# Kernel tuning notes

Measured on AMD Instinct MI355X. Metric: run time of the kernel, lower is better.

The kernel has to match this reference:

```python
import jax, jax.numpy as jnp
import numpy as np

DIM = 768
NUM_HEADS = 12
HEAD_DIM = DIM // NUM_HEADS
SCALE = HEAD_DIM ** -0.5


def setup_inputs() -> dict:
    key = jax.random.key(0)
    k_x, k_qw, k_qb, k_pw, k_pb = jax.random.split(key, 5)
    B, S = 4, 2048
    x = jax.random.normal(k_x, (B, S, DIM), dtype=jnp.float32)
    # torch nn.Linear convention: weight shape [out_features, in_features]
    qkv_w = jax.random.normal(k_qw, (2 * DIM, DIM), dtype=jnp.float32) * 0.02
    qkv_b = jax.random.normal(k_qb, (2 * DIM,), dtype=jnp.float32) * 0.02
    proj_w = jax.random.normal(k_pw, (DIM, DIM), dtype=jnp.float32) * 0.02
    proj_b = jax.random.normal(k_pb, (DIM,), dtype=jnp.float32) * 0.02
    return {"x": x, "qkv_w": qkv_w, "qkv_b": qkv_b, "proj_w": proj_w, "proj_b": proj_b}


def reference(x, qkv_w, qkv_b, proj_w, proj_b):
    B, S, D = x.shape
    H, Hd = NUM_HEADS, HEAD_DIM
    # qkv projection -> (B, S, 2*D)
    qkv = jnp.einsum('bsd,ed->bse', x, qkv_w) + qkv_b
    # reshape to (B, S, 2, H, Hd) then split q, v with heads leading: (B, H, S, Hd)
    qkv = qkv.reshape(B, S, 2, H, Hd).transpose(2, 0, 3, 1, 4)
    q, v = qkv[0], qkv[1]
    q = q * SCALE
    # shared Q=K scores: (B, H, S, S)
    attn = jnp.einsum('bhid,bhjd->bhij', q, q)
    attn = jax.nn.softmax(attn, axis=-1)  # attn_drop p=0 (identity)
    out = jnp.einsum('bhij,bhjd->bhid', attn, v)
    out = out.transpose(0, 2, 1, 3).reshape(B, S, D)
    out = jnp.einsum('bsd,ed->bse', out, proj_w) + proj_b  # proj_drop p=0
    return out
```

## Files before the change

### kernel.cpp

```cpp
#include <hip/hip_runtime.h>
#include <hip/hip_bf16.h>

#define NH 12
#define HD 64
#define SEQ 2048
#define DM 768

typedef __attribute__((ext_vector_type(8))) short bf16x8;
typedef __attribute__((ext_vector_type(4))) short bf16x4;
typedef __attribute__((ext_vector_type(4))) float f32x4;

static __device__ __forceinline__ unsigned short f2bf(float f) {
  unsigned int u = __float_as_uint(f);
  u += 0x7fff + ((u >> 16) & 1);
  return (unsigned short)(u >> 16);
}

static __device__ __forceinline__ unsigned cvt_pk_bf16(float lo, float hi) {
  unsigned r;
  asm("v_cvt_pk_bf16_f32 %0, %1, %2" : "=v"(r) : "v"(lo), "v"(hi));
  return r;
}

static __device__ __forceinline__ void gload_lds16(const void* g, void* l) {
  __builtin_amdgcn_global_load_lds(
      (const __attribute__((address_space(1))) void*)g,
      (__attribute__((address_space(3))) void*)l, 16, 0, 0);
}

static __device__ __forceinline__ f32x4 mfma16(bf16x4 a, bf16x4 b, f32x4 c) {
#if __has_builtin(__builtin_amdgcn_mfma_f32_16x16x16bf16_1k)
  return __builtin_amdgcn_mfma_f32_16x16x16bf16_1k(a, b, c, 0, 0, 0);
#elif __has_builtin(__builtin_amdgcn_mfma_f32_16x16x16_bf16)
  return __builtin_amdgcn_mfma_f32_16x16x16_bf16(a, b, c, 0, 0, 0);
#else
  asm("v_mfma_f32_16x16x16_bf16 %0, %1, %2, %0" : "+v"(c) : "v"(a), "v"(b));
  return c;
#endif
}

#define QSCALE 0.15014030f

__global__ __launch_bounds__(256) void cvt3_kernel(
    const float* __restrict__ s0, unsigned short* __restrict__ d0, int n0,
    const float* __restrict__ s1, unsigned short* __restrict__ d1, int n1,
    const float* __restrict__ s2, unsigned short* __restrict__ d2, int n2) {
  int i = blockIdx.x * 256 + threadIdx.x;
  const int stride = gridDim.x * 256;
  const int ntot = n0 + n1 + n2;
  for (; i < ntot; i += stride) {
    const float* src;
    unsigned short* dst;
    int j = i;
    if (j < n0) { src = s0; dst = d0; }
    else if (j < n0 + n1) { j -= n0; src = s1; dst = d1; }
    else { j -= n0 + n1; src = s2; dst = d2; }
    const float4 a = reinterpret_cast<const float4*>(src)[j * 2];
    const float4 b = reinterpret_cast<const float4*>(src)[j * 2 + 1];
    ushort4 lo = make_ushort4(f2bf(a.x), f2bf(a.y), f2bf(a.z), f2bf(a.w));
    ushort4 hi = make_ushort4(f2bf(b.x), f2bf(b.y), f2bf(b.z), f2bf(b.w));
    reinterpret_cast<ushort4*>(dst)[j * 2] = lo;
    reinterpret_cast<ushort4*>(dst)[j * 2 + 1] = hi;
  }
}

__global__ __launch_bounds__(256) void qkv_kernel(
    const unsigned short* __restrict__ xb, const unsigned short* __restrict__ wb,
    const float* __restrict__ bias,
    unsigned short* __restrict__ qb, unsigned short* __restrict__ vtb) {
  __shared__ alignas(16) char As[2][8192];
  __shared__ alignas(16) char Bs[2][8192];
  const int tid = threadIdx.x;
  const int lane = tid & 63, wid = tid >> 6;
  const int wr = wid >> 1, wc = wid & 1;
  const int g = lane >> 4, c = lane & 15;
  const int m0 = blockIdx.x * 128, n0 = blockIdx.y * 128;
  const char* Ab = (const char*)xb;
  const char* Bb = (const char*)wb;

  const int o0 = tid * 16, o1 = tid * 16 + 4096;
  const int r0 = o0 >> 6, r1 = o1 >> 6;
  const int sw0 = (o0 & 63) ^ (((r0 >> 1) & 3) << 4);
  const int sw1 = (o1 & 63) ^ (((r1 >> 1) & 3) << 4);

  auto stage = [&](int kt, int buf) {
    const int k0b = kt * 64;
    gload_lds16(Ab + (size_t)(m0 + r0) * 1536 + k0b + sw0, &As[buf][o0]);
    gload_lds16(Bb + (size_t)(n0 + r0) * 1536 + k0b + sw0, &Bs[buf][o0]);
    gload_lds16(Ab + (size_t)(m0 + r1) * 1536 + k0b + sw1, &As[buf][o1]);
    gload_lds16(Bb + (size_t)(n0 + r1) * 1536 + k0b + sw1, &Bs[buf][o1]);
  };

  f32x4 acc[4][4] = {};
  stage(0, 0);

  for (int kt = 0; kt < 24; ++kt) {
    __syncthreads();
    if (kt < 23) stage(kt + 1, (kt + 1) & 1);
    const char* Ap = As[kt & 1];
    const char* Bp = Bs[kt & 1];
    bf16x8 a_f[4], b_f[4];
#pragma unroll
    for (int i = 0; i < 4; ++i) {
      const int ra = wr * 64 + i * 16 + c;
      const int rb = wc * 64 + i * 16 + c;
      a_f[i] = *reinterpret_cast<const bf16x8*>(Ap + ra * 64 + ((g ^ ((ra >> 1) & 3)) << 4));
      b_f[i] = *reinterpret_cast<const bf16x8*>(Bp + rb * 64 + ((g ^ ((rb >> 1) & 3)) << 4));
    }
#pragma unroll
    for (int ai = 0; ai < 4; ++ai)
#pragma unroll
      for (int ni = 0; ni < 4; ++ni)
        acc[ai][ni] = __builtin_amdgcn_mfma_f32_16x16x32_bf16(a_f[ai], b_f[ni], acc[ai][ni], 0, 0, 0);
  }

#pragma unroll
  for (int ni = 0; ni < 4; ++ni) {
    const int n = n0 + wc * 64 + ni * 16 + c;
    const float bn = bias[n];
    if (n < DM) {
      const int h = n >> 6, d = n & 63;
#pragma unroll
      for (int ai = 0; ai < 4; ++ai)
#pragma unroll
        for (int r = 0; r < 4; ++r) {
          const int m = m0 + wr * 64 + ai * 16 + g * 4 + r;
          const int bb = m >> 11, s = m & 2047;
          qb[(((size_t)(bb * NH + h)) * SEQ + s) * HD + d] = f2bf((acc[ai][ni][r] + bn) * QSCALE);
        }
    } else {
      const int nn = n - DM;
      const int h = nn >> 6, d = nn & 63;
#pragma unroll
      for (int ai = 0; ai < 4; ++ai) {
        const int m_base = m0 + wr * 64 + ai * 16 + g * 4;
        const int bb = m_base >> 11, s0 = m_base & 2047;
        ushort4 pk = make_ushort4(f2bf(acc[ai][ni][0] + bn), f2bf(acc[ai][ni][1] + bn),
                                  f2bf(acc[ai][ni][2] + bn), f2bf(acc[ai][ni][3] + bn));
        *reinterpret_cast<ushort4*>(
            &vtb[((size_t)(bb * NH + h) * HD + d) * SEQ + s0]) = pk;
      }
    }
  }
}

__global__ __launch_bounds__(256, 4) void attn_kernel(
    const unsigned short* __restrict__ qb, const unsigned short* __restrict__ vtb,
    unsigned short* __restrict__ ao) {
  __shared__ alignas(16) char pool[2][16384];

  const int tid = threadIdx.x;
  const int lane = tid & 63, wid = tid >> 6;
  const int g = lane >> 4, c = lane & 15;
  const int wq = wid >> 1, wk = wid & 1;

  const int wg = blockIdx.x;
  const int xcd = wg & 7;
  const int idx = wg >> 3;
  const int bh = xcd * 6 + (idx >> 5);
  const int qs0 = (idx & 31) * 64;
  const size_t base = (size_t)bh * SEQ * HD;

  bf16x8 qf[2][2];
#pragma unroll
  for (int jq = 0; jq < 2; ++jq) {
    const unsigned short* qrow = &qb[base + (size_t)(qs0 + wq * 32 + jq * 16 + c) * HD + g * 8];
    qf[jq][0] = *reinterpret_cast<const bf16x8*>(qrow);
    qf[jq][1] = *reinterpret_cast<const bf16x8*>(qrow + 32);
  }

  const char* qbB = (const char*)qb;
  const char* vtB = (const char*)vtb;
  const int oK0 = tid * 16, oK1 = tid * 16 + 4096;
  const int swK0 = oK0 ^ (((oK0 >> 7) & 7) << 4);
  const int swK1 = oK1 ^ (((oK1 >> 7) & 7) << 4);
  const int oV0 = tid * 16, oV1 = tid * 16 + 4096;
  const int rV0 = oV0 >> 7, rV1 = oV1 >> 7;
  const int swV0 = (oV0 & 127) ^ (((rV0) & 7) << 4);
  const int swV1 = (oV1 & 127) ^ (((rV1) & 7) << 4);

  auto stage = [&](int t, int buf) {
    char* P = pool[buf];
    const size_t kQ = base * 2 + (size_t)t * 8192;
    gload_lds16(qbB + kQ + swK0, P + oK0);
    gload_lds16(qbB + kQ + swK1, P + oK1);
    gload_lds16(vtB + ((size_t)(bh * HD + rV0) * SEQ + t * 64) * 2 + swV0, P + 8192 + oV0);
    gload_lds16(vtB + ((size_t)(bh * HD + rV1) * SEQ + t * 64) * 2 + swV1, P + 8192 + oV1);
  };

  float l_p[2] = {0.f, 0.f};
  f32x4 o_acc[4][2] = {};

  const int cswz = (c & 7) << 4;

  stage(0, 0);
  asm volatile("s_waitcnt vmcnt(0)" ::: "memory");
  __builtin_amdgcn_sched_barrier(0);
  __builtin_amdgcn_s_barrier();

  for (int t = 0; t < 32; ++t) {
    const char* P = pool[t & 1];
    if (t < 31) stage(t + 1, (t + 1) & 1);

    f32x4 sa[2][2] = {};
    __builtin_amdgcn_s_setprio(1);
#pragma unroll
    for (int jp = 0; jp < 2; ++jp) {
      const int krow = wk * 32 + jp * 16 + c;
      const bf16x8 kf0 = *reinterpret_cast<const bf16x8*>(P + krow * 128 + ((g * 16) ^ cswz));
      const bf16x8 kf1 = *reinterpret_cast<const bf16x8*>(P + krow * 128 + ((64 + g * 16) ^ cswz));
#pragma unroll
      for (int jq = 0; jq < 2; ++jq) {
        sa[jp][jq] = __builtin_amdgcn_mfma_f32_16x16x32_bf16(kf0, qf[jq][0], sa[jp][jq], 0, 0, 0);
        sa[jp][jq] = __builtin_amdgcn_mfma_f32_16x16x32_bf16(kf1, qf[jq][1], sa[jp][jq], 0, 0, 0);
      }
    }
    __builtin_amdgcn_s_setprio(0);

    bf16x4 pb[2][2];
#pragma unroll
    for (int jp = 0; jp < 2; ++jp)
#pragma unroll
      for (int jq = 0; jq < 2; ++jq) {
        float p0 = __builtin_amdgcn_exp2f(sa[jp][jq][0]);
        float p1 = __builtin_amdgcn_exp2f(sa[jp][jq][1]);
        float p2 = __builtin_amdgcn_exp2f(sa[jp][jq][2]);
        float p3 = __builtin_amdgcn_exp2f(sa[jp][jq][3]);
        l_p[jq] += (p0 + p1) + (p2 + p3);
        uint2 wv = make_uint2(cvt_pk_bf16(p0, p1), cvt_pk_bf16(p2, p3));
        pb[jp][jq] = *reinterpret_cast<bf16x4*>(&wv);
      }

    __builtin_amdgcn_s_setprio(1);
#pragma unroll
    for (int dn = 0; dn < 4; ++dn) {
      const int vrow = dn * 16 + c;
      const bf16x4 vf0 = *reinterpret_cast<const bf16x4*>(
          P + 8192 + vrow * 128 + ((wk * 64 + 8 * g) ^ cswz));
      const bf16x4 vf1 = *reinterpret_cast<const bf16x4*>(
          P + 8192 + vrow * 128 + ((wk * 64 + 32 + 8 * g) ^ cswz));
#pragma unroll
      for (int jq = 0; jq < 2; ++jq) {
        o_acc[dn][jq] = mfma16(vf0, pb[0][jq], o_acc[dn][jq]);
        o_acc[dn][jq] = mfma16(vf1, pb[1][jq], o_acc[dn][jq]);
      }
    }
    __builtin_amdgcn_s_setprio(0);

    asm volatile("s_waitcnt vmcnt(0)" ::: "memory");
    __builtin_amdgcn_sched_barrier(0);
    __builtin_amdgcn_s_barrier();
  }

#pragma unroll
  for (int jq = 0; jq < 2; ++jq) {
    float v = l_p[jq];
    v += __shfl_xor(v, 16);
    v += __shfl_xor(v, 32);
    l_p[jq] = v;
  }

  float* ex = (float*)(pool[0] + wq * 16384);
  float* exl = ex + 32 * 68;
  if (wk == 1) {
#pragma unroll
    for (int dn = 0; dn < 4; ++dn)
#pragma unroll
      for (int jq = 0; jq < 2; ++jq)
        *reinterpret_cast<f32x4*>(&ex[(jq * 16 + c) * 68 + dn * 16 + 4 * g]) = o_acc[dn][jq];
    if (g == 0) {
      exl[c] = l_p[0];
      exl[16 + c] = l_p[1];
    }
  }
  __syncthreads();
  if (wk == 0) {
    const int b = bh / NH, h = bh % NH;
    float linv[2];
#pragma unroll
    for (int jq = 0; jq < 2; ++jq)
      linv[jq] = __builtin_amdgcn_rcpf(l_p[jq] + exl[jq * 16 + c]);
#pragma unroll
    for (int dn = 0; dn < 4; ++dn)
#pragma unroll
      for (int jq = 0; jq < 2; ++jq) {
        f32x4 o = o_acc[dn][jq];
        o += *reinterpret_cast<const f32x4*>(&ex[(jq * 16 + c) * 68 + dn * 16 + 4 * g]);
        uint2 wv = make_uint2(cvt_pk_bf16(o[0] * linv[jq], o[1] * linv[jq]),
                              cvt_pk_bf16(o[2] * linv[jq], o[3] * linv[jq]));
        *reinterpret_cast<uint2*>(
            &ao[((size_t)b * SEQ + qs0 + wq * 32 + jq * 16 + c) * DM + h * HD + dn * 16 + 4 * g]) = wv;
      }
  }
}

__global__ __launch_bounds__(256) void proj_kernel(
    const unsigned short* __restrict__ ao, const unsigned short* __restrict__ pwb,
    const float* __restrict__ bias, float* __restrict__ out) {
  __shared__ alignas(16) char As[2][8192];
  __shared__ alignas(16) char Bs[2][8192];
  const int tid = threadIdx.x;
  const int lane = tid & 63, wid = tid >> 6;
  const int wr = wid >> 1, wc = wid & 1;
  const int g = lane >> 4, c = lane & 15;
  const int m0 = blockIdx.x * 128, n0 = blockIdx.y * 128;
  const char* Ab = (const char*)ao;
  const char* Bb = (const char*)pwb;

  const int o0 = tid * 16, o1 = tid * 16 + 4096;
  const int r0 = o0 >> 6, r1 = o1 >> 6;
  const int sw0 = (o0 & 63) ^ (((r0 >> 1) & 3) << 4);
  const int sw1 = (o1 & 63) ^ (((r1 >> 1) & 3) << 4);

  auto stage = [&](int kt, int buf) {
    const int k0b = kt * 64;
    gload_lds16(Ab + (size_t)(m0 + r0) * 1536 + k0b + sw0, &As[buf][o0]);
    gload_lds16(Bb + (size_t)(n0 + r0) * 1536 + k0b + sw0, &Bs[buf][o0]);
    gload_lds16(Ab + (size_t)(m0 + r1) * 1536 + k0b + sw1, &As[buf][o1]);
    gload_lds16(Bb + (size_t)(n0 + r1) * 1536 + k0b + sw1, &Bs[buf][o1]);
  };

  f32x4 acc[4][4] = {};
  stage(0, 0);

  for (int kt = 0; kt < 24; ++kt) {
    __syncthreads();
    if (kt < 23) stage(kt + 1, (kt + 1) & 1);
    const char* Ap = As[kt & 1];
    const char* Bp = Bs[kt & 1];
    bf16x8 a_f[4], b_f[4];
#pragma unroll
    for (int i = 0; i < 4; ++i) {
      const int ra = wr * 64 + i * 16 + c;
      const int rb = wc * 64 + i * 16 + c;
      a_f[i] = *reinterpret_cast<const bf16x8*>(Ap + ra * 64 + ((g ^ ((ra >> 1) & 3)) << 4));
      b_f[i] = *reinterpret_cast<const bf16x8*>(Bp + rb * 64 + ((g ^ ((rb >> 1) & 3)) << 4));
    }
#pragma unroll
    for (int ai = 0; ai < 4; ++ai)
#pragma unroll
      for (int ni = 0; ni < 4; ++ni)
        acc[ai][ni] = __builtin_amdgcn_mfma_f32_16x16x32_bf16(a_f[ai], b_f[ni], acc[ai][ni], 0, 0, 0);
  }

#pragma unroll
  for (int ni = 0; ni < 4; ++ni) {
    const int n = n0 + wc * 64 + ni * 16 + c;
    const float bn = bias[n];
#pragma unroll
    for (int ai = 0; ai < 4; ++ai)
#pragma unroll
      for (int r = 0; r < 4; ++r) {
        const int m = m0 + wr * 64 + ai * 16 + g * 4 + r;
        out[(size_t)m * DM + n] = acc[ai][ni][r] + bn;
      }
  }
}

extern "C" void kernel_launch(void* const* d_in, const int* in_sizes, int n_in,
                              void* d_out, int out_size, void* d_ws, size_t ws_size,
                              hipStream_t stream) {
  const float* x = (const float*)d_in[0];
  const float* qkv_w = (const float*)d_in[1];
  const float* qkv_b = (const float*)d_in[2];
  const float* proj_w = (const float*)d_in[3];
  const float* proj_b = (const float*)d_in[4];
  float* out = (float*)d_out;

  const size_t elems = (size_t)4 * NH * SEQ * HD;
  unsigned short* qbuf = (unsigned short*)d_ws;
  unsigned short* vtbuf = qbuf + elems;
  unsigned short* xbf = vtbuf + elems;
  unsigned short* aobuf = xbf;
  unsigned short* wqkvbf = xbf + elems;
  unsigned short* wprojbf = wqkvbf + (size_t)2 * DM * DM;

  cvt3_kernel<<<dim3(2048), 256, 0, stream>>>(
      x, xbf, (int)(elems / 8),
      qkv_w, wqkvbf, 2 * DM * DM / 8,
      proj_w, wprojbf, DM * DM / 8);

  qkv_kernel<<<dim3(64, 12), 256, 0, stream>>>(xbf, wqkvbf, qkv_b, qbuf, vtbuf);
  attn_kernel<<<dim3(1536), 256, 0, stream>>>(qbuf, vtbuf, aobuf);
  proj_kernel<<<dim3(64, 6), 256, 0, stream>>>(aobuf, wprojbf, proj_b, out);
}
```

Baseline: 132.9 us.

## Split attention key tile across four waves with 512-thread blocks

Doubles the attention block to 512 threads so each wave handles 16 keys of every 64-key tile instead of 32. Each thread now issues one K and one V async load per stage instead of two. The four partial O accumulators and row sums are reduced through LDS in three serialized rounds. This raises wave-level parallelism and memory-issue concurrency per block, at the cost of more barriers in the epilogue and a heavier occupancy constraint from the launch bounds.

```diff
diff --git a/kernel.cpp b/kernel.cpp
--- a/kernel.cpp
+++ b/kernel.cpp
@@ -144,15 +144,16 @@
   }
 }
 
-__global__ __launch_bounds__(256, 4) void attn_kernel(
+__global__ __launch_bounds__(512, 6) void attn_kernel(
     const unsigned short* __restrict__ qb, const unsigned short* __restrict__ vtb,
     unsigned short* __restrict__ ao) {
   __shared__ alignas(16) char pool[2][16384];
+  __shared__ alignas(16) float lsum[4][64];
 
   const int tid = threadIdx.x;
   const int lane = tid & 63, wid = tid >> 6;
   const int g = lane >> 4, c = lane & 15;
-  const int wq = wid >> 1, wk = wid & 1;
+  const int wq = wid >> 2, wk = wid & 3;
 
   const int wg = blockIdx.x;
   const int xcd = wg & 7;
@@ -171,27 +172,22 @@
 
   const char* qbB = (const char*)qb;
   const char* vtB = (const char*)vtb;
-  const int oK0 = tid * 16, oK1 = tid * 16 + 4096;
-  const int swK0 = oK0 ^ (((oK0 >> 7) & 7) << 4);
-  const int swK1 = oK1 ^ (((oK1 >> 7) & 7) << 4);
-  const int oV0 = tid * 16, oV1 = tid * 16 + 4096;
-  const int rV0 = oV0 >> 7, rV1 = oV1 >> 7;
-  const int swV0 = (oV0 & 127) ^ (((rV0) & 7) << 4);
-  const int swV1 = (oV1 & 127) ^ (((rV1) & 7) << 4);
+  const int oT = tid * 16;
+  const int swK = oT ^ (((oT >> 7) & 7) << 4);
+  const int rV = oT >> 7;
+  const int swV = (oT & 127) ^ ((rV & 7) << 4);
 
   auto stage = [&](int t, int buf) {
     char* P = pool[buf];
-    const size_t kQ = base * 2 + (size_t)t * 8192;
-    gload_lds16(qbB + kQ + swK0, P + oK0);
-    gload_lds16(qbB + kQ + swK1, P + oK1);
-    gload_lds16(vtB + ((size_t)(bh * HD + rV0) * SEQ + t * 64) * 2 + swV0, P + 8192 + oV0);
-    gload_lds16(vtB + ((size_t)(bh * HD + rV1) * SEQ + t * 64) * 2 + swV1, P + 8192 + oV1);
+    gload_lds16(qbB + base * 2 + (size_t)t * 8192 + swK, P + oT);
+    gload_lds16(vtB + ((size_t)(bh * HD + rV) * SEQ + t * 64) * 2 + swV, P + 8192 + oT);
   };
 
   float l_p[2] = {0.f, 0.f};
   f32x4 o_acc[4][2] = {};
 
-  const int cswz = (c & 7) << 4;
+  const int krow = wk * 16 + c;
+  const int kswz = (c & 7) << 4;
 
   stage(0, 0);
   asm volatile("s_waitcnt vmcnt(0)" ::: "memory");
@@ -202,48 +198,40 @@
     const char* P = pool[t & 1];
     if (t < 31) stage(t + 1, (t + 1) & 1);
 
-    f32x4 sa[2][2] = {};
-    __builtin_amdgcn_s_setprio(1);
-#pragma unroll
-    for (int jp = 0; jp < 2; ++jp) {
-      const int krow = wk * 32 + jp * 16 + c;
-      const bf16x8 kf0 = *reinterpret_cast<const bf16x8*>(P + krow * 128 + ((g * 16) ^ cswz));
-      const bf16x8 kf1 = *reinterpret_cast<const bf16x8*>(P + krow * 128 + ((64 + g * 16) ^ cswz));
+    f32x4 sa[2] = {};
+    {
+      const bf16x8 kf0 = *reinterpret_cast<const bf16x8*>(P + krow * 128 + ((g * 16) ^ kswz));
+      const bf16x8 kf1 = *reinterpret_cast<const bf16x8*>(P + krow * 128 + ((64 + g * 16) ^ kswz));
+      __builtin_amdgcn_s_setprio(1);
 #pragma unroll
       for (int jq = 0; jq < 2; ++jq) {
-        sa[jp][jq] = __builtin_amdgcn_mfma_f32_16x16x32_bf16(kf0, qf[jq][0], sa[jp][jq], 0, 0, 0);
-        sa[jp][jq] = __builtin_amdgcn_mfma_f32_16x16x32_bf16(kf1, qf[jq][1], sa[jp][jq], 0, 0, 0);
+        sa[jq] = __builtin_amdgcn_mfma_f32_16x16x32_bf16(kf0, qf[jq][0], sa[jq], 0, 0, 0);
+        sa[jq] = __builtin_amdgcn_mfma_f32_16x16x32_bf16(kf1, qf[jq][1], sa[jq], 0, 0, 0);
       }
-    }
-    __builtin_amdgcn_s_setprio(0);
-
-    bf16x4 pb[2][2];
-#pragma unroll
-    for (int jp = 0; jp < 2; ++jp)
-#pragma unroll
-      for (int jq = 0; jq < 2; ++jq) {
-        float p0 = __builtin_amdgcn_exp2f(sa[jp][jq][0]);
-        float p1 = __builtin_amdgcn_exp2f(sa[jp][jq][1]);
-        float p2 = __builtin_amdgcn_exp2f(sa[jp][jq][2]);
-        float p3 = __builtin_amdgcn_exp2f(sa[jp][jq][3]);
-        l_p[jq] += (p0 + p1) + (p2 + p3);
-        uint2 wv = make_uint2(cvt_pk_bf16(p0, p1), cvt_pk_bf16(p2, p3));
-        pb[jp][jq] = *reinterpret_cast<bf16x4*>(&wv);
-      }
+      __builtin_amdgcn_s_setprio(0);
+    }
+
+    bf16x4 pb[2];
+#pragma unroll
+    for (int jq = 0; jq < 2; ++jq) {
+      float p0 = __builtin_amdgcn_exp2f(sa[jq][0]);
+      float p1 = __builtin_amdgcn_exp2f(sa[jq][1]);
+      float p2 = __builtin_amdgcn_exp2f(sa[jq][2]);
+      float p3 = __builtin_amdgcn_exp2f(sa[jq][3]);
+      l_p[jq] += (p0 + p1) + (p2 + p3);
+      uint2 wv = make_uint2(cvt_pk_bf16(p0, p1), cvt_pk_bf16(p2, p3));
+      pb[jq] = *reinterpret_cast<bf16x4*>(&wv);
+    }
 
     __builtin_amdgcn_s_setprio(1);
 #pragma unroll
     for (int dn = 0; dn < 4; ++dn) {
       const int vrow = dn * 16 + c;
-      const bf16x4 vf0 = *reinterpret_cast<const bf16x4*>(
-          P + 8192 + vrow * 128 + ((wk * 64 + 8 * g) ^ cswz));
-      const bf16x4 vf1 = *reinterpret_cast<const bf16x4*>(
-          P + 8192 + vrow * 128 + ((wk * 64 + 32 + 8 * g) ^ cswz));
-#pragma unroll
-      for (int jq = 0; jq < 2; ++jq) {
-        o_acc[dn][jq] = mfma16(vf0, pb[0][jq], o_acc[dn][jq]);
-        o_acc[dn][jq] = mfma16(vf1, pb[1][jq], o_acc[dn][jq]);
-      }
+      const bf16x4 vf = *reinterpret_cast<const bf16x4*>(
+          P + 8192 + vrow * 128 + ((wk * 32 + 8 * g) ^ ((vrow & 7) << 4)));
+#pragma unroll
+      for (int jq = 0; jq < 2; ++jq)
+        o_acc[dn][jq] = mfma16(vf, pb[jq], o_acc[dn][jq]);
     }
     __builtin_amdgcn_s_setprio(0);
 
@@ -258,36 +246,48 @@
     v += __shfl_xor(v, 16);
     v += __shfl_xor(v, 32);
     l_p[jq] = v;
-  }
-
-  float* ex = (float*)(pool[0] + wq * 16384);
-  float* exl = ex + 32 * 68;
-  if (wk == 1) {
+    if (g == 0) lsum[wk][wq * 32 + jq * 16 + c] = v;
+  }
+
+  float* ex = (float*)pool;
+  auto writeO = [&]() {
 #pragma unroll
     for (int dn = 0; dn < 4; ++dn)
 #pragma unroll
       for (int jq = 0; jq < 2; ++jq)
-        *reinterpret_cast<f32x4*>(&ex[(jq * 16 + c) * 68 + dn * 16 + 4 * g]) = o_acc[dn][jq];
-    if (g == 0) {
-      exl[c] = l_p[0];
-      exl[16 + c] = l_p[1];
-    }
-  }
-  __syncthreads();
+        *reinterpret_cast<f32x4*>(
+            &ex[(wq * 32 + jq * 16 + c) * 68 + dn * 16 + 4 * g]) = o_acc[dn][jq];
+  };
+  auto addO = [&]() {
+#pragma unroll
+    for (int dn = 0; dn < 4; ++dn)
+#pragma unroll
+      for (int jq = 0; jq < 2; ++jq)
+        o_acc[dn][jq] += *reinterpret_cast<const f32x4*>(
+            &ex[(wq * 32 + jq * 16 + c) * 68 + dn * 16 + 4 * g]);
+  };
+
+#pragma unroll
+  for (int w = 1; w < 4; ++w) {
+    __syncthreads();
+    if (wk == w) writeO();
+    __syncthreads();
+    if (wk == 0) addO();
+  }
   if (wk == 0) {
     const int b = bh / NH, h = bh % NH;
     float linv[2];
 #pragma unroll
-    for (int jq = 0; jq < 2; ++jq)
-      linv[jq] = __builtin_amdgcn_rcpf(l_p[jq] + exl[jq * 16 + c]);
+    for (int jq = 0; jq < 2; ++jq) {
+      const int q = wq * 32 + jq * 16 + c;
+      linv[jq] = __builtin_amdgcn_rcpf(l_p[jq] + lsum[1][q] + lsum[2][q] + lsum[3][q]);
+    }
 #pragma unroll
     for (int dn = 0; dn < 4; ++dn)
 #pragma unroll
       for (int jq = 0; jq < 2; ++jq) {
-        f32x4 o = o_acc[dn][jq];
-        o += *reinterpret_cast<const f32x4*>(&ex[(jq * 16 + c) * 68 + dn * 16 + 4 * g]);
-        uint2 wv = make_uint2(cvt_pk_bf16(o[0] * linv[jq], o[1] * linv[jq]),
-                              cvt_pk_bf16(o[2] * linv[jq], o[3] * linv[jq]));
+        uint2 wv = make_uint2(cvt_pk_bf16(o_acc[dn][jq][0] * linv[jq], o_acc[dn][jq][1] * linv[jq]),
+                              cvt_pk_bf16(o_acc[dn][jq][2] * linv[jq], o_acc[dn][jq][3] * linv[jq]));
         *reinterpret_cast<uint2*>(
             &ao[((size_t)b * SEQ + qs0 + wq * 32 + jq * 16 + c) * DM + h * HD + dn * 16 + 4 * g]) = wv;
       }
@@ -381,6 +381,6 @@
       proj_w, wprojbf, DM * DM / 8);
 
   qkv_kernel<<<dim3(64, 12), 256, 0, stream>>>(xbf, wqkvbf, qkv_b, qbuf, vtbuf);
-  attn_kernel<<<dim3(1536), 256, 0, stream>>>(qbuf, vtbuf, aobuf);
+  attn_kernel<<<dim3(1536), 512, 0, stream>>>(qbuf, vtbuf, aobuf);
   proj_kernel<<<dim3(64, 6), 256, 0, stream>>>(aobuf, wprojbf, proj_b, out);
 }
```

Result: slower. 137.7 us (+3.6%).

## Use 16x16x32 bf16 MFMA for PV product with permuted V layout

Applied to the files above, without the earlier changes.

Replaces pairs of 16x16x16 bf16 MFMAs in the P·V step with one 16x16x32 MFMA. The V transpose written by the QKV kernel is permuted within 32-element sequence blocks so a single 16-byte LDS read supplies the K=32 operand in the order the concatenated P fragments expect. This halves the MFMA instruction count and the V LDS reads in the inner loop. In exchange, the layout coupling between the two kernels becomes more fragile.

```diff
diff --git a/kernel.cpp b/kernel.cpp
--- a/kernel.cpp
+++ b/kernel.cpp
@@ -28,15 +28,11 @@
       (__attribute__((address_space(3))) void*)l, 16, 0, 0);
 }
 
-static __device__ __forceinline__ f32x4 mfma16(bf16x4 a, bf16x4 b, f32x4 c) {
-#if __has_builtin(__builtin_amdgcn_mfma_f32_16x16x16bf16_1k)
-  return __builtin_amdgcn_mfma_f32_16x16x16bf16_1k(a, b, c, 0, 0, 0);
-#elif __has_builtin(__builtin_amdgcn_mfma_f32_16x16x16_bf16)
-  return __builtin_amdgcn_mfma_f32_16x16x16_bf16(a, b, c, 0, 0, 0);
-#else
-  asm("v_mfma_f32_16x16x16_bf16 %0, %1, %2, %0" : "+v"(c) : "v"(a), "v"(b));
-  return c;
-#endif
+static __device__ __forceinline__ bf16x8 cat4(bf16x4 a, bf16x4 b) {
+  bf16x8 r;
+  r[0] = a[0]; r[1] = a[1]; r[2] = a[2]; r[3] = a[3];
+  r[4] = b[0]; r[5] = b[1]; r[6] = b[2]; r[7] = b[3];
+  return r;
 }
 
 #define QSCALE 0.15014030f
@@ -135,10 +131,12 @@
       for (int ai = 0; ai < 4; ++ai) {
         const int m_base = m0 + wr * 64 + ai * 16 + g * 4;
         const int bb = m_base >> 11, s0 = m_base & 2047;
+        const int blk = s0 >> 5, off = s0 & 31;
+        const int offp = (((off >> 4) & 1) << 2) + (((off >> 2) & 3) << 3);
         ushort4 pk = make_ushort4(f2bf(acc[ai][ni][0] + bn), f2bf(acc[ai][ni][1] + bn),
                                   f2bf(acc[ai][ni][2] + bn), f2bf(acc[ai][ni][3] + bn));
         *reinterpret_cast<ushort4*>(
-            &vtb[((size_t)(bb * NH + h) * HD + d) * SEQ + s0]) = pk;
+            &vtb[((size_t)(bb * NH + h) * HD + d) * SEQ + blk * 32 + offp]) = pk;
       }
     }
   }
@@ -174,18 +172,17 @@
   const int oK0 = tid * 16, oK1 = tid * 16 + 4096;
   const int swK0 = oK0 ^ (((oK0 >> 7) & 7) << 4);
   const int swK1 = oK1 ^ (((oK1 >> 7) & 7) << 4);
-  const int oV0 = tid * 16, oV1 = tid * 16 + 4096;
-  const int rV0 = oV0 >> 7, rV1 = oV1 >> 7;
-  const int swV0 = (oV0 & 127) ^ (((rV0) & 7) << 4);
-  const int swV1 = (oV1 & 127) ^ (((rV1) & 7) << 4);
+  const int rV0 = oK0 >> 7, rV1 = oK1 >> 7;
+  const int swV0 = (oK0 & 127) ^ ((rV0 & 7) << 4);
+  const int swV1 = (oK1 & 127) ^ ((rV1 & 7) << 4);
 
   auto stage = [&](int t, int buf) {
     char* P = pool[buf];
     const size_t kQ = base * 2 + (size_t)t * 8192;
     gload_lds16(qbB + kQ + swK0, P + oK0);
     gload_lds16(qbB + kQ + swK1, P + oK1);
-    gload_lds16(vtB + ((size_t)(bh * HD + rV0) * SEQ + t * 64) * 2 + swV0, P + 8192 + oV0);
-    gload_lds16(vtB + ((size_t)(bh * HD + rV1) * SEQ + t * 64) * 2 + swV1, P + 8192 + oV1);
+    gload_lds16(vtB + ((size_t)(bh * HD + rV0) * SEQ + t * 64) * 2 + swV0, P + 8192 + oK0);
+    gload_lds16(vtB + ((size_t)(bh * HD + rV1) * SEQ + t * 64) * 2 + swV1, P + 8192 + oK1);
   };
 
   float l_p[2] = {0.f, 0.f};
@@ -231,19 +228,18 @@
         pb[jp][jq] = *reinterpret_cast<bf16x4*>(&wv);
       }
 
+    bf16x8 pvv[2];
+    pvv[0] = cat4(pb[0][0], pb[1][0]);
+    pvv[1] = cat4(pb[0][1], pb[1][1]);
     __builtin_amdgcn_s_setprio(1);
 #pragma unroll
     for (int dn = 0; dn < 4; ++dn) {
       const int vrow = dn * 16 + c;
-      const bf16x4 vf0 = *reinterpret_cast<const bf16x4*>(
-          P + 8192 + vrow * 128 + ((wk * 64 + 8 * g) ^ cswz));
-      const bf16x4 vf1 = *reinterpret_cast<const bf16x4*>(
-          P + 8192 + vrow * 128 + ((wk * 64 + 32 + 8 * g) ^ cswz));
-#pragma unroll
-      for (int jq = 0; jq < 2; ++jq) {
-        o_acc[dn][jq] = mfma16(vf0, pb[0][jq], o_acc[dn][jq]);
-        o_acc[dn][jq] = mfma16(vf1, pb[1][jq], o_acc[dn][jq]);
-      }
+      const bf16x8 av = *reinterpret_cast<const bf16x8*>(
+          P + 8192 + vrow * 128 + ((wk * 64 + 16 * g) ^ ((vrow & 7) << 4)));
+#pragma unroll
+      for (int jq = 0; jq < 2; ++jq)
+        o_acc[dn][jq] = __builtin_amdgcn_mfma_f32_16x16x32_bf16(av, pvv[jq], o_acc[dn][jq], 0, 0, 0);
     }
     __builtin_amdgcn_s_setprio(0);
 
```

Result: faster. 124.2 us (-6.5%).
